# Kernel optimization log

Measured on AMD Instinct MI355X. Metric: run time of the kernel, lower is better.

The kernel has to match this reference:

```python
import jax, jax.numpy as jnp
import numpy as np

N_NODES = 50000
EPS_NORM = 1e-12
EPS_ENT = 1e-8

def _l2norm(x):
    # torch.nn.functional.normalize: x / clamp(||x||, min=1e-12)
    n = jnp.sqrt(jnp.sum(x * x, axis=-1, keepdims=True))
    return x / jnp.maximum(n, EPS_NORM)

def _layer(hidden, src, dst, edge_type, multi_emb, proto_emb):
    # hidden: [N,H]; multi_emb: [R,P,H]; proto_emb: [P,H]
    inp_j = hidden[src]                          # [E,H] gather
    rel_basis = multi_emb[edge_type]             # [E,P,H] gather
    sims = jnp.einsum('eh,ph->ep', _l2norm(inp_j), _l2norm(proto_emb))  # cosine sim [E,P]
    proto_proba = jax.nn.softmax(sims, axis=1)   # [E,P]
    msg = jnp.einsum('ep,eph->eh', proto_proba, rel_basis)              # [E,H]
    ent = -jnp.sum(proto_proba * jnp.log(proto_proba + EPS_ENT), axis=1)  # [E]
    logits = -ent
    # scatter_softmax over destination index
    seg_max = jax.ops.segment_max(logits, dst, num_segments=N_NODES)
    ex = jnp.exp(logits - seg_max[dst])
    denom = jax.ops.segment_sum(ex, dst, num_segments=N_NODES)
    attn = ex / denom[dst]                       # [E]
    out = jax.ops.segment_sum(attn[:, None] * msg, dst, num_segments=N_NODES)  # [N,H]
    return out

def setup_inputs() -> dict:
    key = jax.random.key(0)
    ks = jax.random.split(key, 6)
    E = 800000
    H, R, P, L = 128, 18, 18, 3  # num_layers=4 -> 3 NBFCluttr layers
    edge_index = jax.random.randint(ks[0], (2, E), 0, N_NODES, dtype=jnp.int64) if jax.config.read('jax_enable_x64') else jax.random.randint(ks[0], (2, E), 0, N_NODES, dtype=jnp.int32)
    edge_type = jax.random.randint(ks[1], (E,), 0, R, dtype=edge_index.dtype)
    tail_indices = jax.random.randint(ks[2], (1024,), 0, N_NODES, dtype=edge_index.dtype)
    multi_embeddings = jax.random.uniform(ks[3], (L, R, P, H), dtype=jnp.float32)
    proto_embeddings = jax.random.uniform(ks[4], (L, P, H), dtype=jnp.float32)
    source_embedding = jax.random.uniform(ks[5], (H,), dtype=jnp.float32)
    return {"edge_index": edge_index, "edge_type": edge_type, "tail_indices": tail_indices,
            "multi_embeddings": multi_embeddings, "proto_embeddings": proto_embeddings,
            "source_embedding": source_embedding}

def reference(edge_index, edge_type, tail_indices, multi_embeddings, proto_embeddings, source_embedding):
    src, dst = edge_index[0], edge_index[1]
    H = source_embedding.shape[0]
    # boundary condition: source node gets source_embedding, rest zero
    hidden = jnp.zeros((N_NODES, H), dtype=source_embedding.dtype).at[0].set(source_embedding)
    L = multi_embeddings.shape[0]
    for l in range(L):  # small fixed loop over structurally distinct layers
        hidden = _layer(hidden, src, dst, edge_type, multi_embeddings[l], proto_embeddings[l])
    # apply_classifier, eval_mode=True, use_mlp_classifier=False -> cosine sims to last layer prototypes
    out_emb = hidden[tail_indices]               # [B,H]
    sims = jnp.einsum('nh,ph->np', _l2norm(out_emb), _l2norm(proto_embeddings[-1]))
    return sims  # gumbel_softmax_sample with eval_mode=True returns logits unchanged
```

## Files before the change

kernel.cpp:

```cpp
#include <hip/hip_runtime.h>
#include <hip/hip_bf16.h>


#define N_NODES 50000
#define H 128
#define P 18
#define RP 324
#define KPAD 352
#define K0PAD 64
#define ELLW 64
#define NPART 8
#define NODES_PER_PART 6250
#define PREP_MAIN_BLOCKS 384

typedef _Float16 half8 __attribute__((ext_vector_type(8)));
typedef float floatx4 __attribute__((ext_vector_type(4)));

__global__ __launch_bounds__(256) void ell_kernel(const int* __restrict__ src,
                                                  const int* __restrict__ dst,
                                                  const int* __restrict__ etype,
                                                  unsigned* __restrict__ cur,
                                                  unsigned* __restrict__ ep, int E) {
  int part = blockIdx.x & (NPART - 1);
  int base = (blockIdx.x >> 3) * 1024;
  int lo = part * NODES_PER_PART, hi = lo + NODES_PER_PART;
  int i0 = base + threadIdx.x;
  int d[4];
#pragma unroll
  for (int j = 0; j < 4; j++) {
    int i = i0 + j * 256;
    d[j] = (i < E) ? dst[i] : -1;
  }
#pragma unroll
  for (int j = 0; j < 4; j++) {
    if (d[j] >= lo && d[j] < hi) {
      int i = i0 + j * 256;
      unsigned pos = atomicAdd(&cur[d[j]], 1u);
      if (pos < ELLW)
        ep[(size_t)d[j] * ELLW + pos] = (unsigned)src[i] | ((unsigned)etype[i] << 20);
    }
  }
}

__global__ __launch_bounds__(256) void prep_kernel(const float* __restrict__ multi,
                                                   const float* __restrict__ proto,
                                                   const float* __restrict__ semb,
                                                   float* __restrict__ pN,
                                                   _Float16* __restrict__ Btg,
                                                   _Float16* __restrict__ Btl0,
                                                   unsigned* __restrict__ cur) {
  int bid = blockIdx.x;
  if (bid >= PREP_MAIN_BLOCKS) {
    int wave = threadIdx.x >> 6, l = threadIdx.x & 63;
    int row = (bid - PREP_MAIN_BLOCKS) * 4 + wave;
    if (row >= 54) return;
    float a = proto[row * H + l], b = proto[row * H + 64 + l];
    float ss = a * a + b * b;
    for (int m = 32; m > 0; m >>= 1) ss += __shfl_xor(ss, m, 64);
    float inv = 1.f / fmaxf(sqrtf(ss), 1e-12f);
    pN[row * H + l] = a * inv;
    pN[row * H + 64 + l] = b * inv;
    return;
  }
  int idx = bid * 256 + threadIdx.x;
  if (idx < N_NODES) cur[idx] = 0u;
  if (idx < 2 * H * KPAD) {
    int l = idx / (H * KPAD), rem = idx - l * (H * KPAD);
    int h = rem / KPAD, k = rem - h * KPAD;
    const float* B = multi + (size_t)(l + 1) * RP * H;
    Btg[idx] = (k < RP) ? (_Float16)B[k * H + h] : (_Float16)0.f;
    return;
  }
  int idx2 = idx - 2 * H * KPAD;
  if (idx2 >= H * K0PAD) return;
  int h = idx2 >> 6, k = idx2 & 63;
  float s0 = semb[k], s1 = semb[k + 64];
  float ssq = s0 * s0 + s1 * s1;
  float dq[P];
#pragma unroll
  for (int p = 0; p < P; p++) {
    float a = proto[p * H + k], b = proto[p * H + 64 + k];
    float rn = a * a + b * b;
    for (int m = 32; m > 0; m >>= 1) rn += __shfl_xor(rn, m, 64);
    float rinv = 1.f / fmaxf(sqrtf(rn), 1e-12f);
    dq[p] = (s0 * a + s1 * b) * rinv;
  }
  for (int m = 1; m <= 32; m <<= 1) {
    ssq += __shfl_xor(ssq, m, 64);
#pragma unroll
    for (int p = 0; p < P; p++) dq[p] += __shfl_xor(dq[p], m, 64);
  }
  float inv = 1.f / fmaxf(sqrtf(ssq), 1e-12f);
  float sum = 0.f;
#pragma unroll
  for (int p = 0; p < P; p++) {
    dq[p] = __expf(dq[p] * inv - 1.f);
    sum += dq[p];
  }
  float isum = 1.f / sum, ent = 0.f;
#pragma unroll
  for (int p = 0; p < P; p++) {
    dq[p] *= isum;
    ent -= dq[p] * __logf(dq[p] + 1e-8f);
  }
  float w = __expf(-ent);
  float pr = 1.f / 18.f, ent0 = 0.f;
#pragma unroll
  for (int p = 0; p < P; p++) ent0 -= pr * __logf(pr + 1e-8f);
  float qc = __expf(-ent0) * pr;
  float v = 0.f;
  if (k < P) {
#pragma unroll
    for (int p = 0; p < P; p++) v += qc * multi[(k * P + p) * H + h];
  } else if (k < 2 * P) {
    int r = k - P;
#pragma unroll
    for (int p = 0; p < P; p++) v += (w * dq[p] - qc) * multi[(r * P + p) * H + h];
  }
  Btl0[h * K0PAD + k] = (_Float16)v;
}

__global__ __launch_bounds__(256) void hist_kernel(const unsigned* __restrict__ ep,
                                                   const unsigned* __restrict__ cur,
                                                   _Float16* __restrict__ M, int n) {
  int wave = threadIdx.x >> 6, lane = threadIdx.x & 63;
  int nd = blockIdx.x * 4 + wave;
  if (nd >= n) return;
  int cnt = (int)cur[nd];
  if (cnt > ELLW) cnt = ELLW;
  bool a = lane < cnt;
  unsigned pk = a ? ep[(size_t)nd * ELLW + lane] : 0xFFFFFFFFu;
  int r = (int)(pk >> 20);
  unsigned long long zm = __ballot(a && (pk & 0xFFFFFu) == 0u);
  float creg = 0.f, creg0 = 0.f;
#pragma unroll
  for (int rr = 0; rr < P; rr++) {
    unsigned long long m = __ballot(a && (r == rr));
    if (lane == rr) {
      creg = (float)__popcll(m);
      creg0 = (float)__popcll(m & zm);
    }
  }
  int slx = (lane >= P && lane < 2 * P) ? lane - P : 0;
  float v0 = __shfl(creg0, slx, 64);
  float val = (lane < P) ? creg : ((lane < 2 * P) ? v0 : 0.f);
  M[(size_t)nd * K0PAD + lane] = (_Float16)val;
}

__global__ __launch_bounds__(256) void scatter_kernel(const unsigned* __restrict__ ep,
                                                      const unsigned* __restrict__ cur,
                                                      const _Float16* __restrict__ q,
                                                      const int* __restrict__ tl,
                                                      _Float16* __restrict__ M, int n) {
  __shared__ float sl[4][3 * RP];
  int wave = threadIdx.x >> 6, lane = threadIdx.x & 63;
  int t = blockIdx.x * 4 + wave;
  float* s0 = sl[wave];
  for (int i = lane; i < 3 * RP; i += 64) s0[i] = 0.f;
  int sub = lane / 18;
  int j = lane - sub * 18;
  bool act = (sub < 3) && (t < n);
  int cnt = 0;
  size_t b = 0;
  if (t < n) {
    int nd = tl ? tl[t] : t;
    b = (size_t)nd * ELLW;
    cnt = (int)cur[nd];
    if (cnt > ELLW) cnt = ELLW;
  }
  float* ms = s0 + (sub < 3 ? sub : 0) * RP;
  for (int it = 0; it < cnt; it += 9) {
    bool a0 = act && (it + sub < cnt);
    bool a1 = act && (it + 3 + sub < cnt);
    bool a2 = act && (it + 6 + sub < cnt);
    unsigned pk0 = 0, pk1 = 0, pk2 = 0;
    if (a0) pk0 = ep[b + it + sub];
    if (a1) pk1 = ep[b + it + 3 + sub];
    if (a2) pk2 = ep[b + it + 6 + sub];
    float q0 = 0.f, q1 = 0.f, q2 = 0.f;
    if (a0) q0 = (float)q[(size_t)(pk0 & 0xFFFFFu) * P + j];
    if (a1) q1 = (float)q[(size_t)(pk1 & 0xFFFFFu) * P + j];
    if (a2) q2 = (float)q[(size_t)(pk2 & 0xFFFFFu) * P + j];
    if (a0) ms[(pk0 >> 20) * P + j] += q0;
    if (a1) ms[(pk1 >> 20) * P + j] += q1;
    if (a2) ms[(pk2 >> 20) * P + j] += q2;
  }
  if (t < n) {
    for (int k = lane; k < RP; k += 64)
      M[(size_t)t * KPAD + k] = (_Float16)(s0[k] + s0[RP + k] + s0[2 * RP + k]);
    for (int k = RP + lane; k < KPAD; k += 64) M[(size_t)t * KPAD + k] = (_Float16)0.f;
  }
}

template <int MODE>
__global__ __launch_bounds__(256) void gemm_kernel(const _Float16* __restrict__ M,
                                                   const _Float16* __restrict__ Bt,
                                                   const float* __restrict__ pN,
                                                   void* __restrict__ out_ptr, int n,
                                                   int kpad) {
  __shared__ float smem_f[64 * 132];
  _Float16* As = (_Float16*)smem_f;
  _Float16* Bs = (_Float16*)(smem_f + 1024);
  int tid = threadIdx.x;
  int wave = tid >> 6, lane = tid & 63;
  int m15 = lane & 15, quad = lane >> 4;
  int n0 = blockIdx.x * 64;
  floatx4 acc[4][2] = {};

  __shared__ float pns[4 * P * 36];
  for (int i = tid; i < 4 * P * 32; i += 256) {
    int s = i / (P * 32), r = i - s * (P * 32);
    int p = r >> 5, kk = r & 31;
    pns[s * (P * 36) + p * 36 + kk] = pN[p * H + s * 32 + kk];
  }

  for (int kt = 0; kt < (kpad >> 5); kt++) {
    int k0 = kt * 32;
    __syncthreads();
    {
      int row = tid >> 2, kc = (tid & 3) * 8;
      int gr = n0 + row;
      half8 v = {};
      if (gr < n) v = *(const half8*)(M + (size_t)gr * kpad + k0 + kc);
      *(half8*)(As + row * 32 + kc) = v;
    }
    {
      int col = tid >> 1, kc = (tid & 1) * 16;
      const _Float16* srcp = Bt + (size_t)col * kpad + k0 + kc;
      *(half8*)(Bs + col * 32 + kc) = *(const half8*)srcp;
      *(half8*)(Bs + col * 32 + kc + 8) = *(const half8*)(srcp + 8);
    }
    __syncthreads();
    half8 bfrag0 = *(const half8*)(Bs + (wave * 32 + m15) * 32 + quad * 8);
    half8 bfrag1 = *(const half8*)(Bs + (wave * 32 + 16 + m15) * 32 + quad * 8);
#pragma unroll
    for (int mt = 0; mt < 4; mt++) {
      half8 afrag = *(const half8*)(As + (mt * 16 + m15) * 32 + quad * 8);
      acc[mt][0] = __builtin_amdgcn_mfma_f32_16x16x32_f16(afrag, bfrag0, acc[mt][0], 0, 0, 0);
      acc[mt][1] = __builtin_amdgcn_mfma_f32_16x16x32_f16(afrag, bfrag1, acc[mt][1], 0, 0, 0);
    }
  }
  __syncthreads();
#pragma unroll
  for (int mt = 0; mt < 4; mt++)
#pragma unroll
    for (int c = 0; c < 2; c++)
#pragma unroll
      for (int reg = 0; reg < 4; reg++)
        smem_f[(mt * 16 + quad * 4 + reg) * 132 + wave * 32 + c * 16 + m15] = acc[mt][c][reg];
  __syncthreads();
  int node = tid >> 2, sub = tid & 3;
  int gnode = n0 + node;
  const float* trow = smem_f + node * 132 + sub * 32;
  const float* ps = pns + sub * (P * 36);
  float ss = 0.f;
  float dot[P];
#pragma unroll
  for (int p = 0; p < P; p++) dot[p] = 0.f;
#pragma unroll
  for (int k4 = 0; k4 < 8; k4++) {
    float4 y = *(const float4*)(trow + k4 * 4);
    ss += y.x * y.x + y.y * y.y + y.z * y.z + y.w * y.w;
#pragma unroll
    for (int p = 0; p < P; p++) {
      float4 b = *(const float4*)(ps + p * 36 + k4 * 4);
      dot[p] += y.x * b.x + y.y * b.y + y.z * b.z + y.w * b.w;
    }
  }
  for (int m = 1; m <= 2; m <<= 1) {
    ss += __shfl_xor(ss, m, 64);
#pragma unroll
    for (int p = 0; p < P; p++) dot[p] += __shfl_xor(dot[p], m, 64);
  }
  if (gnode < n) {
    float inv = 1.f / fmaxf(sqrtf(ss), 1e-12f);
    if (MODE == 1) {
      float* outp = (float*)out_ptr;
      for (int p = sub; p < P; p += 4) outp[(size_t)gnode * P + p] = dot[p] * inv;
    } else {
      float sum = 0.f;
#pragma unroll
      for (int p = 0; p < P; p++) {
        dot[p] = __expf(dot[p] * inv - 1.f);
        sum += dot[p];
      }
      float isum = 1.f / sum, ent = 0.f;
#pragma unroll
      for (int p = 0; p < P; p++) {
        dot[p] *= isum;
        ent -= dot[p] * __logf(dot[p] + 1e-8f);
      }
      float w = __expf(-ent);
      _Float16* qp = (_Float16*)out_ptr;
      for (int p = sub; p < P; p += 4) qp[(size_t)gnode * P + p] = (_Float16)(w * dot[p]);
    }
  }
}

extern "C" void kernel_launch(void* const* d_in, const int* in_sizes, int n_in,
                              void* d_out, int out_size, void* d_ws, size_t ws_size,
                              hipStream_t stream) {
  const int* eidx = (const int*)d_in[0];
  int E = in_sizes[0] / 2;
  const int* src = eidx;
  const int* dst = eidx + E;
  const int* etype = (const int*)d_in[1];
  const int* tails = (const int*)d_in[2];
  int T = in_sizes[2];
  const float* multi = (const float*)d_in[3];
  const float* proto = (const float*)d_in[4];
  const float* semb = (const float*)d_in[5];
  float* out = (float*)d_out;

  char* w = (char*)d_ws;
  auto alloc = [&](size_t bytes) {
    char* p = w;
    w += (bytes + 255) & ~(size_t)255;
    return p;
  };
  _Float16* q = (_Float16*)alloc((size_t)N_NODES * P * 2);
  float* pNs = (float*)alloc((size_t)3 * P * H * 4);
  _Float16* Mg = (_Float16*)alloc((size_t)N_NODES * KPAD * 2);
  _Float16* Btg = (_Float16*)alloc((size_t)2 * H * KPAD * 2);
  _Float16* Btl0 = (_Float16*)alloc((size_t)H * K0PAD * 2);
  unsigned* cur = (unsigned*)alloc((size_t)N_NODES * 4);
  unsigned* ep = (unsigned*)alloc((size_t)N_NODES * ELLW * 4);

  prep_kernel<<<PREP_MAIN_BLOCKS + 14, 256, 0, stream>>>(multi, proto, semb, pNs, Btg,
                                                         Btl0, cur);

  int eb4 = (E + 1023) / 1024;
  ell_kernel<<<eb4 * NPART, 256, 0, stream>>>(src, dst, etype, cur, ep, E);

  hist_kernel<<<(N_NODES + 3) / 4, 256, 0, stream>>>(ep, cur, Mg, N_NODES);
  gemm_kernel<0><<<(N_NODES + 63) / 64, 256, 0, stream>>>(Mg, Btl0, pNs + (size_t)1 * P * H, q,
                                                          N_NODES, K0PAD);

  scatter_kernel<<<(N_NODES + 3) / 4, 256, 0, stream>>>(ep, cur, q, nullptr, Mg, N_NODES);
  gemm_kernel<0><<<(N_NODES + 63) / 64, 256, 0, stream>>>(Mg, Btg, pNs + (size_t)2 * P * H, q,
                                                          N_NODES, KPAD);

  scatter_kernel<<<(T + 3) / 4, 256, 0, stream>>>(ep, cur, q, tails, Mg, T);
  gemm_kernel<1><<<(T + 63) / 64, 256, 0, stream>>>(Mg, Btg + (size_t)H * KPAD,
                                                    pNs + (size_t)2 * P * H, out, T, KPAD);
}
```

Before: 238.5 us.

## Move source-node edge corrections into sparse patch kernel and halve layer-0 K

Layer 0 no longer builds a 64-wide histogram that counts edges from node 0 separately. The ELL build records the few edges whose source is node 0 in a small list. A single-wave patch kernel then recomputes q for just those destination nodes, which lets the dense layer-0 GEMM run with K=32 instead of 64. The ELL kernel handles one edge per thread, scatter is unrolled 6 ways, and its output is written as half2. The risk is a serial single-wave patch kernel with quadratic deduplication, and silently wrong results if more than 1024 edges leave node 0.

```diff
diff --git a/kernel.cpp b/kernel.cpp
--- a/kernel.cpp
+++ b/kernel.cpp
@@ -7,38 +7,37 @@
 #define P 18
 #define RP 324
 #define KPAD 352
-#define K0PAD 64
+#define K0PAD 32
 #define ELLW 64
 #define NPART 8
 #define NODES_PER_PART 6250
 #define PREP_MAIN_BLOCKS 384
+#define N0CAP 1024
 
 typedef _Float16 half8 __attribute__((ext_vector_type(8)));
+typedef _Float16 half2v __attribute__((ext_vector_type(2)));
 typedef float floatx4 __attribute__((ext_vector_type(4)));
 
 __global__ __launch_bounds__(256) void ell_kernel(const int* __restrict__ src,
                                                   const int* __restrict__ dst,
                                                   const int* __restrict__ etype,
                                                   unsigned* __restrict__ cur,
-                                                  unsigned* __restrict__ ep, int E) {
+                                                  unsigned* __restrict__ ep,
+                                                  unsigned* __restrict__ n0list, int E) {
   int part = blockIdx.x & (NPART - 1);
-  int base = (blockIdx.x >> 3) * 1024;
-  int lo = part * NODES_PER_PART, hi = lo + NODES_PER_PART;
-  int i0 = base + threadIdx.x;
-  int d[4];
-#pragma unroll
-  for (int j = 0; j < 4; j++) {
-    int i = i0 + j * 256;
-    d[j] = (i < E) ? dst[i] : -1;
-  }
-#pragma unroll
-  for (int j = 0; j < 4; j++) {
-    if (d[j] >= lo && d[j] < hi) {
-      int i = i0 + j * 256;
-      unsigned pos = atomicAdd(&cur[d[j]], 1u);
-      if (pos < ELLW)
-        ep[(size_t)d[j] * ELLW + pos] = (unsigned)src[i] | ((unsigned)etype[i] << 20);
-    }
+  int i = (blockIdx.x >> 3) * 256 + threadIdx.x;
+  if (i >= E) return;
+  int d = dst[i];
+  int lo = part * NODES_PER_PART;
+  if (d < lo || d >= lo + NODES_PER_PART) return;
+  int s = src[i];
+  int r = etype[i];
+  unsigned pos = atomicAdd(&cur[d], 1u);
+  if (pos < ELLW)
+    ep[(size_t)d * ELLW + pos] = (unsigned)s | ((unsigned)r << 20);
+  if (s == 0) {
+    unsigned ix = atomicAdd(&cur[N_NODES], 1u);
+    if (ix < N0CAP) n0list[ix] = (unsigned)d | ((unsigned)r << 20);
   }
 }
 
@@ -48,6 +47,7 @@
                                                    float* __restrict__ pN,
                                                    _Float16* __restrict__ Btg,
                                                    _Float16* __restrict__ Btl0,
+                                                   _Float16* __restrict__ BtD,
                                                    unsigned* __restrict__ cur) {
   int bid = blockIdx.x;
   if (bid >= PREP_MAIN_BLOCKS) {
@@ -63,7 +63,7 @@
     return;
   }
   int idx = bid * 256 + threadIdx.x;
-  if (idx < N_NODES) cur[idx] = 0u;
+  if (idx <= N_NODES) cur[idx] = 0u;
   if (idx < 2 * H * KPAD) {
     int l = idx / (H * KPAD), rem = idx - l * (H * KPAD);
     int h = rem / KPAD, k = rem - h * KPAD;
@@ -72,7 +72,7 @@
     return;
   }
   int idx2 = idx - 2 * H * KPAD;
-  if (idx2 >= H * K0PAD) return;
+  if (idx2 >= H * 64) return;
   int h = idx2 >> 6, k = idx2 & 63;
   float s0 = semb[k], s1 = semb[k + 64];
   float ssq = s0 * s0 + s1 * s1;
@@ -108,16 +108,20 @@
 #pragma unroll
   for (int p = 0; p < P; p++) ent0 -= pr * __logf(pr + 1e-8f);
   float qc = __expf(-ent0) * pr;
-  float v = 0.f;
-  if (k < P) {
-#pragma unroll
-    for (int p = 0; p < P; p++) v += qc * multi[(k * P + p) * H + h];
-  } else if (k < 2 * P) {
-    int r = k - P;
+  if (k < K0PAD) {
+    float v = 0.f;
+    if (k < P) {
+#pragma unroll
+      for (int p = 0; p < P; p++) v += qc * multi[(k * P + p) * H + h];
+    }
+    Btl0[h * K0PAD + k] = (_Float16)v;
+  } else if (k < K0PAD + P) {
+    int r = k - K0PAD;
+    float v = 0.f;
 #pragma unroll
     for (int p = 0; p < P; p++) v += (w * dq[p] - qc) * multi[(r * P + p) * H + h];
-  }
-  Btl0[h * K0PAD + k] = (_Float16)v;
+    BtD[r * H + h] = (_Float16)v;
+  }
 }
 
 __global__ __launch_bounds__(256) void hist_kernel(const unsigned* __restrict__ ep,
@@ -131,20 +135,71 @@
   bool a = lane < cnt;
   unsigned pk = a ? ep[(size_t)nd * ELLW + lane] : 0xFFFFFFFFu;
   int r = (int)(pk >> 20);
-  unsigned long long zm = __ballot(a && (pk & 0xFFFFFu) == 0u);
-  float creg = 0.f, creg0 = 0.f;
+  float creg = 0.f;
 #pragma unroll
   for (int rr = 0; rr < P; rr++) {
     unsigned long long m = __ballot(a && (r == rr));
-    if (lane == rr) {
-      creg = (float)__popcll(m);
-      creg0 = (float)__popcll(m & zm);
-    }
-  }
-  int slx = (lane >= P && lane < 2 * P) ? lane - P : 0;
-  float v0 = __shfl(creg0, slx, 64);
-  float val = (lane < P) ? creg : ((lane < 2 * P) ? v0 : 0.f);
-  M[(size_t)nd * K0PAD + lane] = (_Float16)val;
+    if (lane == rr) creg = (float)__popcll(m);
+  }
+  if (lane < K0PAD) M[(size_t)nd * K0PAD + lane] = (_Float16)creg;
+}
+
+__global__ __launch_bounds__(64) void patch_kernel(const unsigned* __restrict__ cur,
+                                                   const unsigned* __restrict__ n0list,
+                                                   const _Float16* __restrict__ M,
+                                                   const _Float16* __restrict__ Btl0,
+                                                   const _Float16* __restrict__ BtD,
+                                                   const float* __restrict__ pN,
+                                                   _Float16* __restrict__ q) {
+  int n0 = (int)cur[N_NODES];
+  if (n0 > N0CAP) n0 = N0CAP;
+  int lane = threadIdx.x;
+  for (int e = 0; e < n0; e++) {
+    unsigned pe = n0list[e];
+    int d = (int)(pe & 0xFFFFFu);
+    bool first = true;
+    for (int e2 = 0; e2 < e; e2++)
+      if ((int)(n0list[e2] & 0xFFFFFu) == d) { first = false; break; }
+    if (!first) continue;
+    float ya = 0.f, yb = 0.f;
+#pragma unroll
+    for (int r = 0; r < P; r++) {
+      float c = (float)M[(size_t)d * K0PAD + r];
+      ya += c * (float)Btl0[lane * K0PAD + r];
+      yb += c * (float)Btl0[(lane + 64) * K0PAD + r];
+    }
+    for (int e2 = e; e2 < n0; e2++) {
+      unsigned p2 = n0list[e2];
+      if ((int)(p2 & 0xFFFFFu) != d) continue;
+      int r2 = (int)(p2 >> 20);
+      ya += (float)BtD[r2 * H + lane];
+      yb += (float)BtD[r2 * H + lane + 64];
+    }
+    float ss = ya * ya + yb * yb;
+    float dot[P];
+#pragma unroll
+    for (int p = 0; p < P; p++) dot[p] = ya * pN[p * H + lane] + yb * pN[p * H + lane + 64];
+    for (int m = 1; m <= 32; m <<= 1) {
+      ss += __shfl_xor(ss, m, 64);
+#pragma unroll
+      for (int p = 0; p < P; p++) dot[p] += __shfl_xor(dot[p], m, 64);
+    }
+    float inv = 1.f / fmaxf(sqrtf(ss), 1e-12f);
+    float sum = 0.f;
+#pragma unroll
+    for (int p = 0; p < P; p++) {
+      dot[p] = __expf(dot[p] * inv - 1.f);
+      sum += dot[p];
+    }
+    float isum = 1.f / sum, ent = 0.f;
+#pragma unroll
+    for (int p = 0; p < P; p++) {
+      dot[p] *= isum;
+      ent -= dot[p] * __logf(dot[p] + 1e-8f);
+    }
+    float w = __expf(-ent);
+    if (lane < P) q[(size_t)d * P + lane] = (_Float16)(w * dot[lane]);
+  }
 }
 
 __global__ __launch_bounds__(256) void scatter_kernel(const unsigned* __restrict__ ep,
@@ -169,26 +224,37 @@
     if (cnt > ELLW) cnt = ELLW;
   }
   float* ms = s0 + (sub < 3 ? sub : 0) * RP;
-  for (int it = 0; it < cnt; it += 9) {
-    bool a0 = act && (it + sub < cnt);
-    bool a1 = act && (it + 3 + sub < cnt);
-    bool a2 = act && (it + 6 + sub < cnt);
-    unsigned pk0 = 0, pk1 = 0, pk2 = 0;
-    if (a0) pk0 = ep[b + it + sub];
-    if (a1) pk1 = ep[b + it + 3 + sub];
-    if (a2) pk2 = ep[b + it + 6 + sub];
-    float q0 = 0.f, q1 = 0.f, q2 = 0.f;
-    if (a0) q0 = (float)q[(size_t)(pk0 & 0xFFFFFu) * P + j];
-    if (a1) q1 = (float)q[(size_t)(pk1 & 0xFFFFFu) * P + j];
-    if (a2) q2 = (float)q[(size_t)(pk2 & 0xFFFFFu) * P + j];
-    if (a0) ms[(pk0 >> 20) * P + j] += q0;
-    if (a1) ms[(pk1 >> 20) * P + j] += q1;
-    if (a2) ms[(pk2 >> 20) * P + j] += q2;
+  for (int it = 0; it < cnt; it += 18) {
+    bool aa[6];
+    unsigned pk[6];
+    float qv[6];
+#pragma unroll
+    for (int u = 0; u < 6; u++) {
+      int e = it + 3 * u + sub;
+      aa[u] = act && (e < cnt);
+      pk[u] = aa[u] ? ep[b + e] : 0u;
+    }
+#pragma unroll
+    for (int u = 0; u < 6; u++)
+      qv[u] = aa[u] ? (float)q[(size_t)(pk[u] & 0xFFFFFu) * P + j] : 0.f;
+#pragma unroll
+    for (int u = 0; u < 6; u++)
+      if (aa[u]) ms[(pk[u] >> 20) * P + j] += qv[u];
   }
   if (t < n) {
-    for (int k = lane; k < RP; k += 64)
-      M[(size_t)t * KPAD + k] = (_Float16)(s0[k] + s0[RP + k] + s0[2 * RP + k]);
-    for (int k = RP + lane; k < KPAD; k += 64) M[(size_t)t * KPAD + k] = (_Float16)0.f;
+    for (int wd = lane; wd < RP / 2; wd += 64) {
+      float2 x0 = *(const float2*)(s0 + 2 * wd);
+      float2 x1 = *(const float2*)(s0 + RP + 2 * wd);
+      float2 x2 = *(const float2*)(s0 + 2 * RP + 2 * wd);
+      half2v hv;
+      hv[0] = (_Float16)(x0.x + x1.x + x2.x);
+      hv[1] = (_Float16)(x0.y + x1.y + x2.y);
+      *(half2v*)(M + (size_t)t * KPAD + 2 * wd) = hv;
+    }
+    for (int wd = RP / 2 + lane; wd < KPAD / 2; wd += 64) {
+      half2v z = {};
+      *(half2v*)(M + (size_t)t * KPAD + 2 * wd) = z;
+    }
   }
 }
 
@@ -323,18 +389,22 @@
   _Float16* Mg = (_Float16*)alloc((size_t)N_NODES * KPAD * 2);
   _Float16* Btg = (_Float16*)alloc((size_t)2 * H * KPAD * 2);
   _Float16* Btl0 = (_Float16*)alloc((size_t)H * K0PAD * 2);
-  unsigned* cur = (unsigned*)alloc((size_t)N_NODES * 4);
+  _Float16* BtD = (_Float16*)alloc((size_t)P * H * 2);
+  unsigned* cur = (unsigned*)alloc((size_t)(N_NODES + 1) * 4);
+  unsigned* n0list = (unsigned*)alloc((size_t)N0CAP * 4);
   unsigned* ep = (unsigned*)alloc((size_t)N_NODES * ELLW * 4);
 
+  int eb = (E + 255) / 256;
+
   prep_kernel<<<PREP_MAIN_BLOCKS + 14, 256, 0, stream>>>(multi, proto, semb, pNs, Btg,
-                                                         Btl0, cur);
-
-  int eb4 = (E + 1023) / 1024;
-  ell_kernel<<<eb4 * NPART, 256, 0, stream>>>(src, dst, etype, cur, ep, E);
+                                                         Btl0, BtD, cur);
+
+  ell_kernel<<<eb * NPART, 256, 0, stream>>>(src, dst, etype, cur, ep, n0list, E);
 
   hist_kernel<<<(N_NODES + 3) / 4, 256, 0, stream>>>(ep, cur, Mg, N_NODES);
   gemm_kernel<0><<<(N_NODES + 63) / 64, 256, 0, stream>>>(Mg, Btl0, pNs + (size_t)1 * P * H, q,
                                                           N_NODES, K0PAD);
+  patch_kernel<<<1, 64, 0, stream>>>(cur, n0list, Mg, Btl0, BtD, pNs + (size_t)1 * P * H, q);
 
   scatter_kernel<<<(N_NODES + 3) / 4, 256, 0, stream>>>(ep, cur, q, nullptr, Mg, N_NODES);
   gemm_kernel<0><<<(N_NODES + 63) / 64, 256, 0, stream>>>(Mg, Btg, pNs + (size_t)2 * P * H, q,
```

New measurement: 301.4 us. +26.4%, slower.
